# Optimization experiments

Hardware: AMD Instinct MI355X
Metric: run time of the kernel (lower is better)

## Reference

```python
import jax, jax.numpy as jnp
import numpy as np

N = 50000
E = 800000
HID = 128
H = 4
C = HID // H  # 32
ED = 4


def setup_inputs() -> dict:
    key = jax.random.key(0)
    ks = jax.random.split(key, 16)
    s = 0.05
    rn = lambda k, shape: jax.random.normal(k, shape, jnp.float32) * s
    z = lambda n: jnp.zeros((n,), jnp.float32)
    return {
        'x': jax.random.normal(ks[0], (N, HID), jnp.float32),
        'edge_index': jax.random.randint(ks[1], (2, E), 0, N, dtype=jnp.int32),
        'edge_attr': jax.random.normal(ks[2], (E, ED), jnp.float32),
        'ln1_g': jnp.ones((HID,), jnp.float32), 'ln1_b': z(HID),
        'Wq': rn(ks[3], (HID, HID)), 'bq': z(HID),
        'Wk': rn(ks[4], (HID, HID)), 'bk': z(HID),
        'Wv': rn(ks[5], (HID, HID)), 'bv': z(HID),
        'We': rn(ks[6], (HID, ED)),
        'Wskip': rn(ks[7], (HID, HID)), 'bskip': z(HID),
        'Wbeta': rn(ks[8], (1, 3 * HID)),
        'ln2_g': jnp.ones((HID,), jnp.float32), 'ln2_b': z(HID),
        'W1': rn(ks[9], (4 * HID, HID)), 'b1': z(4 * HID),
        'W2': rn(ks[10], (HID, 4 * HID)), 'b2': z(HID),
    }


def layer_norm(x, g, b, eps=1e-5):
    mu = jnp.mean(x, axis=-1, keepdims=True)
    var = jnp.mean(jnp.square(x - mu), axis=-1, keepdims=True)
    return (x - mu) * jax.lax.rsqrt(var + eps) * g + b


def transformer_conv(h, edge_index, edge_attr, Wq, bq, Wk, bk, Wv, bv, We, Wskip, bskip, Wbeta):
    src, dst = edge_index[0], edge_index[1]
    n = h.shape[0]
    q = (h @ Wq.T + bq).reshape(n, H, C)
    k = (h @ Wk.T + bk).reshape(n, H, C)
    v = (h @ Wv.T + bv).reshape(n, H, C)
    e = (edge_attr @ We.T).reshape(-1, H, C)  # [E,H,C]
    k_j = k[src] + e
    v_j = v[src] + e
    alpha = jnp.einsum('ehc,ehc->eh', q[dst], k_j) / np.sqrt(C)  # [E,H]
    # segment softmax over destination nodes
    m = jax.ops.segment_max(alpha, dst, num_segments=n)  # [N,H]
    a = jnp.exp(alpha - m[dst])
    denom = jax.ops.segment_sum(a, dst, num_segments=n) + 1e-16
    a = a / denom[dst]
    out = jax.ops.segment_sum(a[:, :, None] * v_j, dst, num_segments=n)  # [N,H,C]
    out = out.reshape(n, H * C)
    skip = h @ Wskip.T + bskip
    beta = jax.nn.sigmoid(jnp.concatenate([out, skip, out - skip], axis=-1) @ Wbeta.T)  # [N,1]
    return beta * skip + (1.0 - beta) * out


def reference(x, edge_index, edge_attr, ln1_g, ln1_b, Wq, bq, Wk, bk, Wv, bv, We, Wskip, bskip, Wbeta, ln2_g, ln2_b, W1, b1, W2, b2):
    h = transformer_conv(layer_norm(x, ln1_g, ln1_b), edge_index, edge_attr,
                         Wq, bq, Wk, bk, Wv, bv, We, Wskip, bskip, Wbeta)
    x = x + h
    h2 = layer_norm(x, ln2_g, ln2_b)
    h2 = jax.nn.relu(h2 @ W1.T + b1) @ W2.T + b2
    return x + h2
```

## Files before the change

kernel.cpp:

```cpp
#include <hip/hip_runtime.h>

#define N_NODES 50000
#define E_EDGES 800000
#define HID 128
#define NQB 782
#define SCAN_BLK 1024
#define NSB 49
#define WCB 192

typedef __attribute__((ext_vector_type(8))) short short8;
typedef __attribute__((ext_vector_type(4))) float f32x4;

static __device__ __forceinline__ unsigned short f2bf(float f) {
  unsigned int u = __builtin_bit_cast(unsigned int, f);
  u += 0x7fff + ((u >> 16) & 1);
  return (unsigned short)(u >> 16);
}
static __device__ __forceinline__ float bf2f(unsigned short u) {
  return __builtin_bit_cast(float, (unsigned int)u << 16);
}
static __device__ __forceinline__ unsigned short pk_fp8(float a, float b) {
  return (unsigned short)(__builtin_amdgcn_cvt_pk_fp8_f32(a, b, 0, false) & 0xffff);
}

__global__ __launch_bounds__(256) void wcvt_kernel(
    const float4* __restrict__ Wq, const float4* __restrict__ Wk,
    const float4* __restrict__ Wv, const float4* __restrict__ Ws,
    const float4* __restrict__ W1, const float4* __restrict__ W2,
    unsigned short* __restrict__ wqkvs, unsigned short* __restrict__ w1b,
    unsigned short* __restrict__ w2b, int* __restrict__ deg)
{
  if (blockIdx.x >= WCB) {
    int idx = ((blockIdx.x - WCB) * 256 + threadIdx.x) * 4;
    if (idx + 3 < N_NODES) *(int4*)(deg + idx) = (int4){0, 0, 0, 0};
    else {
      for (int t = 0; t < 4; t++)
        if (idx + t < N_NODES) deg[idx + t] = 0;
    }
    return;
  }
  int i = blockIdx.x * 256 + threadIdx.x;
  const float4* src;
  unsigned short* dst;
  if (i < 16384) {
    int part = i >> 12;
    src = ((part == 0) ? Wq : (part == 1) ? Wk : (part == 2) ? Wv : Ws) + (i & 4095);
    dst = wqkvs + i * 4;
  } else if (i < 32768) {
    src = W1 + (i - 16384); dst = w1b + (size_t)(i - 16384) * 4;
  } else {
    src = W2 + (i - 32768); dst = w2b + (size_t)(i - 32768) * 4;
  }
  float4 v = *src;
  ushort4 o;
  o.x = f2bf(v.x); o.y = f2bf(v.y); o.z = f2bf(v.z); o.w = f2bf(v.w);
  *(ushort4*)dst = o;
}

__global__ __launch_bounds__(256) void qkvs_kernel(
    const float* __restrict__ x,
    const float* __restrict__ g1, const float* __restrict__ bln,
    const unsigned short* __restrict__ wqkvs,
    const float* __restrict__ bq, const float* __restrict__ bk,
    const float* __restrict__ bv, const float* __restrict__ bs,
    unsigned short* __restrict__ qb, unsigned char* __restrict__ kvb,
    unsigned short* __restrict__ sb,
    const int* __restrict__ ei, int* __restrict__ deg, int n)
{
  if (blockIdx.x >= NQB) {
    for (int e = (blockIdx.x - NQB) * 256 + threadIdx.x; e < E_EDGES;
         e += NQB * 256)
      atomicAdd(deg + ei[E_EDGES + e], 1);
    return;
  }
  __shared__ short lnA[64][128];
  int node0 = blockIdx.x * 64;
  int tid = threadIdx.x;
  int g = tid >> 4, gl = tid & 15, c0 = gl * 8;
  {
    float gv[8], bv2[8];
    *(float4*)&gv[0] = *(const float4*)(g1 + c0);
    *(float4*)&gv[4] = *(const float4*)(g1 + c0 + 4);
    *(float4*)&bv2[0] = *(const float4*)(bln + c0);
    *(float4*)&bv2[4] = *(const float4*)(bln + c0 + 4);
    for (int ni = 0; ni < 4; ni++) {
      int nl = ni * 16 + g;
      int node = node0 + nl;
      short8 h8 = {0, 0, 0, 0, 0, 0, 0, 0};
      if (node < n) {
        float vals[8];
        const float* row = x + (size_t)node * HID + c0;
        *(float4*)&vals[0] = *(const float4*)row;
        *(float4*)&vals[4] = *(const float4*)(row + 4);
        float sum = 0.f;
        #pragma unroll
        for (int j = 0; j < 8; j++) sum += vals[j];
        sum += __shfl_xor(sum, 8); sum += __shfl_xor(sum, 4);
        sum += __shfl_xor(sum, 2); sum += __shfl_xor(sum, 1);
        float mu = sum * (1.f / 128.f);
        float sq = 0.f;
        #pragma unroll
        for (int j = 0; j < 8; j++) { float d = vals[j] - mu; sq += d * d; }
        sq += __shfl_xor(sq, 8); sq += __shfl_xor(sq, 4);
        sq += __shfl_xor(sq, 2); sq += __shfl_xor(sq, 1);
        float rstd = rsqrtf(sq * (1.f / 128.f) + 1e-5f);
        #pragma unroll
        for (int j = 0; j < 8; j++)
          h8[j] = (short)f2bf((vals[j] - mu) * rstd * gv[j] + bv2[j]);
      }
      *(short8*)&lnA[nl][(gl ^ (nl & 7)) * 8] = h8;
    }
  }
  __syncthreads();
  int w = tid >> 6, lane = tid & 63;
  int lg = lane >> 4, ll = lane & 15;
  short8 bfr[4][4];
  #pragma unroll
  for (int nt = 0; nt < 4; nt++) {
    int arow = nt * 16 + ll;
    #pragma unroll
    for (int kt = 0; kt < 4; kt++)
      bfr[nt][kt] = *(const short8*)&lnA[arow][((kt * 4 + lg) ^ (ll & 7)) * 8];
  }
  const float* biasp = (w == 0) ? bq : (w == 1) ? bk : (w == 2) ? bv : bs;
  bool ok[4];
  #pragma unroll
  for (int nt = 0; nt < 4; nt++) ok[nt] = (node0 + nt * 16 + ll) < n;
  for (int ci = 0; ci < 8; ci++) {
    const unsigned short* wrow = wqkvs + (size_t)(w * 128 + ci * 16 + ll) * 128 + lg * 8;
    short8 af[4];
    #pragma unroll
    for (int kt = 0; kt < 4; kt++) af[kt] = *(const short8*)(wrow + kt * 32);
    f32x4 acc[4];
    #pragma unroll
    for (int nt = 0; nt < 4; nt++) acc[nt] = (f32x4){0.f, 0.f, 0.f, 0.f};
    #pragma unroll
    for (int kt = 0; kt < 4; kt++)
      #pragma unroll
      for (int nt = 0; nt < 4; nt++)
        acc[nt] = __builtin_amdgcn_mfma_f32_16x16x32_bf16(af[kt], bfr[nt][kt], acc[nt], 0, 0, 0);
    int jj = ci * 16 + lg * 4;
    float4 bq4 = *(const float4*)(biasp + jj);
    #pragma unroll
    for (int nt = 0; nt < 4; nt++) {
      if (!ok[nt]) continue;
      int node = node0 + nt * 16 + ll;
      float v0 = acc[nt][0] + bq4.x, v1 = acc[nt][1] + bq4.y;
      float v2 = acc[nt][2] + bq4.z, v3 = acc[nt][3] + bq4.w;
      if (w == 0 || w == 3) {
        ushort4 o;
        o.x = f2bf(v0); o.y = f2bf(v1); o.z = f2bf(v2); o.w = f2bf(v3);
        *(ushort4*)((w == 0 ? qb : sb) + (size_t)node * HID + jj) = o;
      } else {
        unsigned word = (unsigned)pk_fp8(v0, v1) | ((unsigned)pk_fp8(v2, v3) << 16);
        *(unsigned*)(kvb + (unsigned)node * 256 + (jj >> 2) * 8 + (w == 1 ? 0 : 4)) = word;
      }
    }
  }
}

__global__ __launch_bounds__(256) void scan1_kernel(
    const int* __restrict__ deg, int* __restrict__ bsum)
{
  __shared__ int wsum[4];
  int b = blockIdx.x;
  int idx = b * SCAN_BLK + threadIdx.x * 4;
  int4 v = {0, 0, 0, 0};
  if (idx + 3 < N_NODES) v = *(const int4*)(deg + idx);
  else {
    if (idx     < N_NODES) v.x = deg[idx];
    if (idx + 1 < N_NODES) v.y = deg[idx + 1];
    if (idx + 2 < N_NODES) v.z = deg[idx + 2];
    if (idx + 3 < N_NODES) v.w = deg[idx + 3];
  }
  int s = v.x + v.y + v.z + v.w;
  for (int m = 1; m < 64; m <<= 1) s += __shfl_xor(s, m);
  int lane = threadIdx.x & 63, w = threadIdx.x >> 6;
  if (lane == 0) wsum[w] = s;
  __syncthreads();
  if (threadIdx.x == 0) bsum[b] = wsum[0] + wsum[1] + wsum[2] + wsum[3];
}

__global__ __launch_bounds__(256) void scan2_kernel(
    const int* __restrict__ deg, const int* __restrict__ bsum,
    int* __restrict__ row_start, int* __restrict__ cursor)
{
  __shared__ int boff_s;
  __shared__ int wsum[4];
  int b = blockIdx.x;
  int tid = threadIdx.x;
  int lane = tid & 63, w = tid >> 6;
  if (tid < 64) {
    int v = (lane < b) ? bsum[lane] : 0;
    for (int m = 1; m < 64; m <<= 1) v += __shfl_xor(v, m);
    if (lane == 0) boff_s = v;
  }
  int idx = b * SCAN_BLK + tid * 4;
  int4 v = {0, 0, 0, 0};
  if (idx + 3 < N_NODES) v = *(const int4*)(deg + idx);
  else {
    if (idx     < N_NODES) v.x = deg[idx];
    if (idx + 1 < N_NODES) v.y = deg[idx + 1];
    if (idx + 2 < N_NODES) v.z = deg[idx + 2];
    if (idx + 3 < N_NODES) v.w = deg[idx + 3];
  }
  int ts = v.x + v.y + v.z + v.w;
  int incl = ts;
  for (int m = 1; m < 64; m <<= 1) {
    int t = __shfl_up(incl, m);
    if (lane >= m) incl += t;
  }
  if (lane == 63) wsum[w] = incl;
  __syncthreads();
  int woff = 0;
  for (int i = 0; i < w; i++) woff += wsum[i];
  int excl = boff_s + woff + incl - ts;
  int4 o;
  o.x = excl;
  o.y = excl + v.x;
  o.z = excl + v.x + v.y;
  o.w = excl + v.x + v.y + v.z;
  if (idx + 3 < N_NODES) {
    *(int4*)(row_start + idx) = o;
    *(int4*)(cursor + idx) = o;
  } else {
    if (idx     < N_NODES) { row_start[idx]     = o.x; cursor[idx]     = o.x; }
    if (idx + 1 < N_NODES) { row_start[idx + 1] = o.y; cursor[idx + 1] = o.y; }
    if (idx + 2 < N_NODES) { row_start[idx + 2] = o.z; cursor[idx + 2] = o.z; }
    if (idx + 3 < N_NODES) { row_start[idx + 3] = o.w; cursor[idx + 3] = o.w; }
  }
}

__global__ __launch_bounds__(256) void scatter_kernel(
    const int* __restrict__ ei, const float4* __restrict__ attr,
    int* __restrict__ cursor,
    int* __restrict__ csr_src, float4* __restrict__ csr_attr)
{
  int e = blockIdx.x * 256 + threadIdx.x;
  if (e >= E_EDGES) return;
  int dst = ei[E_EDGES + e];
  int pos = atomicAdd(cursor + dst, 1);
  csr_src[pos] = ei[e] * 256;
  csr_attr[pos] = attr[e];
}

__global__ __launch_bounds__(256) void gather_kernel(
    const int* __restrict__ row_start, const int* __restrict__ deg,
    const int* __restrict__ csr_src, const float4* __restrict__ csr_attr,
    const float* __restrict__ We,
    const unsigned short* __restrict__ qb, const unsigned char* __restrict__ kvb,
    const float* __restrict__ x, const unsigned short* __restrict__ sb,
    const float* __restrict__ Wb, unsigned short* __restrict__ xnb, int n)
{
  int node = (blockIdx.x * blockDim.x + threadIdx.x) >> 6;
  if (node >= n) return;
  int lane = threadIdx.x & 63;
  int hl = lane & 31;
  int s  = lane >> 5;
  int c0 = hl * 4;
  ushort4 q4 = *(const ushort4*)(qb + (size_t)node * HID + c0);
  float q0 = bf2f(q4.x), q1 = bf2f(q4.y), q2 = bf2f(q4.z), q3 = bf2f(q4.w);
  float4 wr0 = *(const float4*)(We + (c0 + 0) * 4);
  float4 wr1 = *(const float4*)(We + (c0 + 1) * 4);
  float4 wr2 = *(const float4*)(We + (c0 + 2) * 4);
  float4 wr3 = *(const float4*)(We + (c0 + 3) * 4);
  float qwe0 = q0 * wr0.x + q1 * wr1.x + q2 * wr2.x + q3 * wr3.x;
  float qwe1 = q0 * wr0.y + q1 * wr1.y + q2 * wr2.y + q3 * wr3.y;
  float qwe2 = q0 * wr0.z + q1 * wr1.z + q2 * wr2.z + q3 * wr3.z;
  float qwe3 = q0 * wr0.w + q1 * wr1.w + q2 * wr2.w + q3 * wr3.w;
  qwe0 += __shfl_xor(qwe0, 1); qwe0 += __shfl_xor(qwe0, 2); qwe0 += __shfl_xor(qwe0, 4);
  qwe1 += __shfl_xor(qwe1, 1); qwe1 += __shfl_xor(qwe1, 2); qwe1 += __shfl_xor(qwe1, 4);
  qwe2 += __shfl_xor(qwe2, 1); qwe2 += __shfl_xor(qwe2, 2); qwe2 += __shfl_xor(qwe2, 4);
  qwe3 += __shfl_xor(qwe3, 1); qwe3 += __shfl_xor(qwe3, 2); qwe3 += __shfl_xor(qwe3, 4);
  const float s2 = 0.17677669529663687f * 1.4426950408889634f;
  float q0s = q0 * s2, q1s = q1 * s2, q2s = q2 * s2, q3s = q3 * s2;
  qwe0 *= s2; qwe1 *= s2; qwe2 *= s2; qwe3 *= s2;
  float acc0 = 0.f, acc1 = 0.f, acc2 = 0.f, acc3 = 0.f, den = 0.f;
  float aat0 = 0.f, aat1 = 0.f, aat2 = 0.f, aat3 = 0.f;
  int rs = row_start[node];
  int cnt = deg[node];
  int re = rs + cnt;
  unsigned off = (unsigned)hl * 8;
  uint2 kvc = {0u, 0u};
  float4 ac = {0.f, 0.f, 0.f, 0.f};
  {
    int jj = rs + s;
    if (jj < re) {
      kvc = *(const uint2*)(kvb + (unsigned)csr_src[jj] + off);
      ac = csr_attr[jj];
    }
  }
  for (int j = rs; j < re; j += 2) {
    uint2 kvn = {0u, 0u};
    float4 an = {0.f, 0.f, 0.f, 0.f};
    int jn = j + 2 + s;
    if (jn < re) {
      kvn = *(const uint2*)(kvb + (unsigned)csr_src[jn] + off);
      an = csr_attr[jn];
    }
    float dot = q0s * __builtin_amdgcn_cvt_f32_fp8((int)kvc.x, 0) +
                q1s * __builtin_amdgcn_cvt_f32_fp8((int)kvc.x, 1) +
                q2s * __builtin_amdgcn_cvt_f32_fp8((int)kvc.x, 2) +
                q3s * __builtin_amdgcn_cvt_f32_fp8((int)kvc.x, 3);
    dot += __shfl_xor(dot, 1);
    dot += __shfl_xor(dot, 2);
    dot += __shfl_xor(dot, 4);
    float e = exp2f(dot + qwe0 * ac.x + qwe1 * ac.y + qwe2 * ac.z + qwe3 * ac.w);
    e = (j + s < re) ? e : 0.f;
    den += e;
    aat0 += e * ac.x; aat1 += e * ac.y;
    aat2 += e * ac.z; aat3 += e * ac.w;
    acc0 += e * __builtin_amdgcn_cvt_f32_fp8((int)kvc.y, 0);
    acc1 += e * __builtin_amdgcn_cvt_f32_fp8((int)kvc.y, 1);
    acc2 += e * __builtin_amdgcn_cvt_f32_fp8((int)kvc.y, 2);
    acc3 += e * __builtin_amdgcn_cvt_f32_fp8((int)kvc.y, 3);
    kvc = kvn; ac = an;
  }
  acc0 += __shfl_xor(acc0, 32); acc1 += __shfl_xor(acc1, 32);
  acc2 += __shfl_xor(acc2, 32); acc3 += __shfl_xor(acc3, 32);
  den  += __shfl_xor(den, 32);
  aat0 += __shfl_xor(aat0, 32); aat1 += __shfl_xor(aat1, 32);
  aat2 += __shfl_xor(aat2, 32); aat3 += __shfl_xor(aat3, 32);
  float inv = 1.0f / (den + 1e-16f);
  float o0 = (acc0 + wr0.x * aat0 + wr0.y * aat1 + wr0.z * aat2 + wr0.w * aat3) * inv;
  float o1 = (acc1 + wr1.x * aat0 + wr1.y * aat1 + wr1.z * aat2 + wr1.w * aat3) * inv;
  float o2 = (acc2 + wr2.x * aat0 + wr2.y * aat1 + wr2.z * aat2 + wr2.w * aat3) * inv;
  float o3 = (acc3 + wr3.x * aat0 + wr3.y * aat1 + wr3.z * aat2 + wr3.w * aat3) * inv;
  ushort4 sp4 = *(const ushort4*)(sb + (size_t)node * HID + c0);
  float sk0 = bf2f(sp4.x), sk1 = bf2f(sp4.y), sk2 = bf2f(sp4.z), sk3 = bf2f(sp4.w);
  float4 wbA = *(const float4*)(Wb + c0);
  float4 wbB = *(const float4*)(Wb + 128 + c0);
  float4 wbC = *(const float4*)(Wb + 256 + c0);
  float bpart = o0 * (wbA.x + wbC.x) + sk0 * (wbB.x - wbC.x) +
                o1 * (wbA.y + wbC.y) + sk1 * (wbB.y - wbC.y) +
                o2 * (wbA.z + wbC.z) + sk2 * (wbB.z - wbC.z) +
                o3 * (wbA.w + wbC.w) + sk3 * (wbB.w - wbC.w);
  bpart += __shfl_xor(bpart, 1); bpart += __shfl_xor(bpart, 2);
  bpart += __shfl_xor(bpart, 4); bpart += __shfl_xor(bpart, 8);
  bpart += __shfl_xor(bpart, 16);
  float beta = 1.0f / (1.0f + exp2f(-bpart * 1.4426950408889634f));
  if (lane < 32) {
    float4 xv = *(const float4*)(x + (size_t)node * HID + c0);
    ushort4 o4;
    o4.x = f2bf(xv.x + beta * sk0 + (1.0f - beta) * o0);
    o4.y = f2bf(xv.y + beta * sk1 + (1.0f - beta) * o1);
    o4.z = f2bf(xv.z + beta * sk2 + (1.0f - beta) * o2);
    o4.w = f2bf(xv.w + beta * sk3 + (1.0f - beta) * o3);
    *(ushort4*)(xnb + (size_t)node * HID + c0) = o4;
  }
}

__global__ __launch_bounds__(256) void mlp_kernel(
    const unsigned short* __restrict__ xnb,
    const float* __restrict__ g2, const float* __restrict__ b2ln,
    const unsigned short* __restrict__ w1b, const float* __restrict__ b1,
    const unsigned short* __restrict__ w2b, const float* __restrict__ b2,
    float* __restrict__ out, int n)
{
  __shared__ short lnA[32][128];
  __shared__ short tS[32][512];
  short* tsf = &tS[0][0];
  int node0 = blockIdx.x * 32;
  int tid = threadIdx.x;
  int g = tid >> 4, gl = tid & 15, c0 = gl * 8;
  {
    float gv[8], bv2[8];
    *(float4*)&gv[0] = *(const float4*)(g2 + c0);
    *(float4*)&gv[4] = *(const float4*)(g2 + c0 + 4);
    *(float4*)&bv2[0] = *(const float4*)(b2ln + c0);
    *(float4*)&bv2[4] = *(const float4*)(b2ln + c0 + 4);
    for (int ni = 0; ni < 2; ni++) {
      int nl = ni * 16 + g;
      int node = node0 + nl;
      short8 h8 = {0, 0, 0, 0, 0, 0, 0, 0};
      if (node < n) {
        short8 raw = *(const short8*)(xnb + (size_t)node * HID + c0);
        float vals[8];
        #pragma unroll
        for (int j = 0; j < 8; j++) vals[j] = bf2f((unsigned short)raw[j]);
        float sum = 0.f;
        #pragma unroll
        for (int j = 0; j < 8; j++) sum += vals[j];
        sum += __shfl_xor(sum, 8); sum += __shfl_xor(sum, 4);
        sum += __shfl_xor(sum, 2); sum += __shfl_xor(sum, 1);
        float mu = sum * (1.f / 128.f);
        float sq = 0.f;
        #pragma unroll
        for (int j = 0; j < 8; j++) { float d = vals[j] - mu; sq += d * d; }
        sq += __shfl_xor(sq, 8); sq += __shfl_xor(sq, 4);
        sq += __shfl_xor(sq, 2); sq += __shfl_xor(sq, 1);
        float rstd = rsqrtf(sq * (1.f / 128.f) + 1e-5f);
        #pragma unroll
        for (int j = 0; j < 8; j++)
          h8[j] = (short)f2bf((vals[j] - mu) * rstd * gv[j] + bv2[j]);
      }
      *(short8*)&lnA[nl][(gl ^ (nl & 7)) * 8] = h8;
    }
  }
  __syncthreads();
  int w = tid >> 6, lane = tid & 63;
  int lg = lane >> 4, ll = lane & 15;
  int swz = (ll & 7) << 1;
  bool ok0 = (node0 + ll) < n, ok1 = (node0 + 16 + ll) < n;
  {
    short8 bfr1[2][4];
    #pragma unroll
    for (int nt = 0; nt < 2; nt++) {
      int arow = nt * 16 + ll;
      #pragma unroll
      for (int kt = 0; kt < 4; kt++)
        bfr1[nt][kt] = *(const short8*)&lnA[arow][((kt * 4 + lg) ^ (ll & 7)) * 8];
    }
    for (int ji = 0; ji < 8; ji++) {
      int jt = w * 8 + ji;
      const unsigned short* wrow = w1b + (size_t)(jt * 16 + ll) * 128 + lg * 8;
      short8 af[4];
      #pragma unroll
      for (int kt = 0; kt < 4; kt++) af[kt] = *(const short8*)(wrow + kt * 32);
      f32x4 acc[2];
      acc[0] = (f32x4){0.f, 0.f, 0.f, 0.f};
      acc[1] = (f32x4){0.f, 0.f, 0.f, 0.f};
      #pragma unroll
      for (int kt = 0; kt < 4; kt++) {
        acc[0] = __builtin_amdgcn_mfma_f32_16x16x32_bf16(af[kt], bfr1[0][kt], acc[0], 0, 0, 0);
        acc[1] = __builtin_amdgcn_mfma_f32_16x16x32_bf16(af[kt], bfr1[1][kt], acc[1], 0, 0, 0);
      }
      float4 bj = *(const float4*)(b1 + jt * 16 + lg * 4);
      int gr = jt * 4 + lg;
      #pragma unroll
      for (int nt = 0; nt < 2; nt++) {
        int nl = nt * 16 + ll;
        ushort4 o;
        o.x = f2bf(fmaxf(acc[nt][0] + bj.x, 0.f));
        o.y = f2bf(fmaxf(acc[nt][1] + bj.y, 0.f));
        o.z = f2bf(fmaxf(acc[nt][2] + bj.z, 0.f));
        o.w = f2bf(fmaxf(acc[nt][3] + bj.w, 0.f));
        *(ushort4*)&tsf[nl * 512 + (gr ^ swz) * 4] = o;
      }
    }
  }
  __syncthreads();
  {
    for (int ci = 0; ci < 2; ci++) {
      int ct = w * 2 + ci;
      f32x4 acc[2];
      acc[0] = (f32x4){0.f, 0.f, 0.f, 0.f};
      acc[1] = (f32x4){0.f, 0.f, 0.f, 0.f};
      const unsigned short* wrow = w2b + (size_t)(ct * 16 + ll) * 512 + lg * 8;
      #pragma unroll
      for (int kt = 0; kt < 16; kt++) {
        short8 af = *(const short8*)(wrow + kt * 32);
        int G = kt * 8 + lg * 2;
        short8 b0 = *(const short8*)&tsf[(0 * 16 + ll) * 512 + (G ^ swz) * 4];
        short8 b1f = *(const short8*)&tsf[(1 * 16 + ll) * 512 + (G ^ swz) * 4];
        acc[0] = __builtin_amdgcn_mfma_f32_16x16x32_bf16(af, b0, acc[0], 0, 0, 0);
        acc[1] = __builtin_amdgcn_mfma_f32_16x16x32_bf16(af, b1f, acc[1], 0, 0, 0);
      }
      int c = ct * 16 + lg * 4;
      float4 b2q = *(const float4*)(b2 + c);
      #pragma unroll
      for (int nt = 0; nt < 2; nt++) {
        if (nt == 0 ? !ok0 : !ok1) continue;
        int node = node0 + nt * 16 + ll;
        ushort4 xr = *(const ushort4*)(xnb + (size_t)node * HID + c);
        float4 o;
        o.x = bf2f(xr.x) + acc[nt][0] + b2q.x;
        o.y = bf2f(xr.y) + acc[nt][1] + b2q.y;
        o.z = bf2f(xr.z) + acc[nt][2] + b2q.z;
        o.w = bf2f(xr.w) + acc[nt][3] + b2q.w;
        *(float4*)(out + (size_t)node * HID + c) = o;
      }
    }
  }
}

extern "C" void kernel_launch(void* const* d_in, const int* in_sizes, int n_in,
                              void* d_out, int out_size, void* d_ws, size_t ws_size,
                              hipStream_t stream) {
  const float* x     = (const float*)d_in[0];
  const int*   ei    = (const int*)d_in[1];
  const float* attr  = (const float*)d_in[2];
  const float* ln1_g = (const float*)d_in[3];
  const float* ln1_b = (const float*)d_in[4];
  const float* Wq    = (const float*)d_in[5];
  const float* bq    = (const float*)d_in[6];
  const float* Wk    = (const float*)d_in[7];
  const float* bk    = (const float*)d_in[8];
  const float* Wv    = (const float*)d_in[9];
  const float* bv    = (const float*)d_in[10];
  const float* We    = (const float*)d_in[11];
  const float* Wskip = (const float*)d_in[12];
  const float* bskip = (const float*)d_in[13];
  const float* Wbeta = (const float*)d_in[14];
  const float* ln2_g = (const float*)d_in[15];
  const float* ln2_b = (const float*)d_in[16];
  const float* W1    = (const float*)d_in[17];
  const float* b1    = (const float*)d_in[18];
  const float* W2    = (const float*)d_in[19];
  const float* b2    = (const float*)d_in[20];
  float* out = (float*)d_out;
  float* ws  = (float*)d_ws;

  size_t NH  = (size_t)N_NODES * HID;
  size_t NHf = NH / 2;
  unsigned short* sb  = (unsigned short*)ws;
  unsigned short* xnb = (unsigned short*)(ws + NHf);
  unsigned short* qb  = (unsigned short*)(ws + 2 * NHf);
  unsigned char*  kvb = (unsigned char*)(ws + 3 * NHf);
  float* base2 = ws + 3 * NHf + (size_t)N_NODES * 256 / 4;
  int* deg       = (int*)base2;
  int* row_start = deg + N_NODES;
  int* cursor    = row_start + N_NODES;
  int* csr_src   = cursor + N_NODES;
  float4* csr_attr = (float4*)(base2 + 950000);
  unsigned short* wqkvs = (unsigned short*)(base2 + 950000 + (size_t)E_EDGES * 4);
  unsigned short* w1b   = wqkvs + 65536;
  unsigned short* w2b   = w1b + 65536;
  int* bsum = (int*)(w2b + 65536);

  wcvt_kernel<<<WCB + NSB, 256, 0, stream>>>(
      (const float4*)Wq, (const float4*)Wk, (const float4*)Wv,
      (const float4*)Wskip, (const float4*)W1, (const float4*)W2,
      wqkvs, w1b, w2b, deg);
  qkvs_kernel<<<2 * NQB, 256, 0, stream>>>(
      x, ln1_g, ln1_b, wqkvs, bq, bk, bv, bskip, qb, kvb, sb, ei, deg, N_NODES);
  scan1_kernel<<<NSB, 256, 0, stream>>>(deg, bsum);
  scan2_kernel<<<NSB, 256, 0, stream>>>(deg, bsum, row_start, cursor);
  scatter_kernel<<<(E_EDGES + 255) / 256, 256, 0, stream>>>(
      ei, (const float4*)attr, cursor, csr_src, csr_attr);
  gather_kernel<<<(N_NODES * 64 + 255) / 256, 256, 0, stream>>>(
      row_start, deg, csr_src, csr_attr, We, qb, kvb, x, sb, Wbeta, xnb, N_NODES);
  mlp_kernel<<<(N_NODES + 31) / 32, 256, 0, stream>>>(
      xnb, ln2_g, ln2_b, w1b, b1, w2b, b2, out, N_NODES);
}
```

Measured before the change: 248.8 us.

## Process four edges per wave with 16-lane groups and interleaved 8-channel KV layout

Changes the fp8 K/V buffer layout so each lane's 8 K channels and 8 V channels sit in one contiguous 16-byte chunk. The gather kernel now splits each wave into four 16-lane groups, each handling one edge with a 16-byte load and packed fp8 conversions. The goal is to raise memory-level parallelism per wave, cut loop iterations and the shuffle depth of the per-edge dot product. In exchange each lane holds more registers, and the final reductions across the edge groups need extra shuffles.

Result: slower. 297.3 us (+19.5%).

```diff
diff --git a/kernel.cpp b/kernel.cpp
--- a/kernel.cpp
+++ b/kernel.cpp
@@ -10,6 +10,7 @@
 
 typedef __attribute__((ext_vector_type(8))) short short8;
 typedef __attribute__((ext_vector_type(4))) float f32x4;
+typedef __attribute__((ext_vector_type(2))) float f32x2;
 
 static __device__ __forceinline__ unsigned short f2bf(float f) {
   unsigned int u = __builtin_bit_cast(unsigned int, f);
@@ -153,7 +154,8 @@
         *(ushort4*)((w == 0 ? qb : sb) + (size_t)node * HID + jj) = o;
       } else {
         unsigned word = (unsigned)pk_fp8(v0, v1) | ((unsigned)pk_fp8(v2, v3) << 16);
-        *(unsigned*)(kvb + (unsigned)node * 256 + (jj >> 2) * 8 + (w == 1 ? 0 : 4)) = word;
+        *(unsigned*)(kvb + (unsigned)node * 256 + (jj >> 3) * 16 + (jj & 7) +
+                     (w == 1 ? 0 : 8)) = word;
       }
     }
   }
@@ -255,98 +257,110 @@
   int node = (blockIdx.x * blockDim.x + threadIdx.x) >> 6;
   if (node >= n) return;
   int lane = threadIdx.x & 63;
-  int hl = lane & 31;
-  int s  = lane >> 5;
-  int c0 = hl * 4;
-  ushort4 q4 = *(const ushort4*)(qb + (size_t)node * HID + c0);
-  float q0 = bf2f(q4.x), q1 = bf2f(q4.y), q2 = bf2f(q4.z), q3 = bf2f(q4.w);
-  float4 wr0 = *(const float4*)(We + (c0 + 0) * 4);
-  float4 wr1 = *(const float4*)(We + (c0 + 1) * 4);
-  float4 wr2 = *(const float4*)(We + (c0 + 2) * 4);
-  float4 wr3 = *(const float4*)(We + (c0 + 3) * 4);
-  float qwe0 = q0 * wr0.x + q1 * wr1.x + q2 * wr2.x + q3 * wr3.x;
-  float qwe1 = q0 * wr0.y + q1 * wr1.y + q2 * wr2.y + q3 * wr3.y;
-  float qwe2 = q0 * wr0.z + q1 * wr1.z + q2 * wr2.z + q3 * wr3.z;
-  float qwe3 = q0 * wr0.w + q1 * wr1.w + q2 * wr2.w + q3 * wr3.w;
-  qwe0 += __shfl_xor(qwe0, 1); qwe0 += __shfl_xor(qwe0, 2); qwe0 += __shfl_xor(qwe0, 4);
-  qwe1 += __shfl_xor(qwe1, 1); qwe1 += __shfl_xor(qwe1, 2); qwe1 += __shfl_xor(qwe1, 4);
-  qwe2 += __shfl_xor(qwe2, 1); qwe2 += __shfl_xor(qwe2, 2); qwe2 += __shfl_xor(qwe2, 4);
-  qwe3 += __shfl_xor(qwe3, 1); qwe3 += __shfl_xor(qwe3, 2); qwe3 += __shfl_xor(qwe3, 4);
+  int hl = lane & 15;
+  int s  = lane >> 4;
+  int c0 = hl * 8;
+  short8 q8r = *(const short8*)(qb + (size_t)node * HID + c0);
+  float qv[8];
+  #pragma unroll
+  for (int i = 0; i < 8; i++) qv[i] = bf2f((unsigned short)q8r[i]);
+  float qwe0 = 0.f, qwe1 = 0.f, qwe2 = 0.f, qwe3 = 0.f;
+  #pragma unroll
+  for (int i = 0; i < 8; i++) {
+    float4 wr = *(const float4*)(We + (c0 + i) * 4);
+    qwe0 += qv[i] * wr.x; qwe1 += qv[i] * wr.y;
+    qwe2 += qv[i] * wr.z; qwe3 += qv[i] * wr.w;
+  }
+  qwe0 += __shfl_xor(qwe0, 1); qwe0 += __shfl_xor(qwe0, 2);
+  qwe1 += __shfl_xor(qwe1, 1); qwe1 += __shfl_xor(qwe1, 2);
+  qwe2 += __shfl_xor(qwe2, 1); qwe2 += __shfl_xor(qwe2, 2);
+  qwe3 += __shfl_xor(qwe3, 1); qwe3 += __shfl_xor(qwe3, 2);
   const float s2 = 0.17677669529663687f * 1.4426950408889634f;
-  float q0s = q0 * s2, q1s = q1 * s2, q2s = q2 * s2, q3s = q3 * s2;
+  float qs[8];
+  #pragma unroll
+  for (int i = 0; i < 8; i++) qs[i] = qv[i] * s2;
   qwe0 *= s2; qwe1 *= s2; qwe2 *= s2; qwe3 *= s2;
-  float acc0 = 0.f, acc1 = 0.f, acc2 = 0.f, acc3 = 0.f, den = 0.f;
+  float acc[8] = {0.f, 0.f, 0.f, 0.f, 0.f, 0.f, 0.f, 0.f};
+  float den = 0.f;
   float aat0 = 0.f, aat1 = 0.f, aat2 = 0.f, aat3 = 0.f;
   int rs = row_start[node];
   int cnt = deg[node];
   int re = rs + cnt;
-  unsigned off = (unsigned)hl * 8;
-  uint2 kvc = {0u, 0u};
+  unsigned off = (unsigned)hl * 16;
+  uint4 kvc = {0u, 0u, 0u, 0u};
   float4 ac = {0.f, 0.f, 0.f, 0.f};
   {
     int jj = rs + s;
     if (jj < re) {
-      kvc = *(const uint2*)(kvb + (unsigned)csr_src[jj] + off);
+      kvc = *(const uint4*)(kvb + (unsigned)csr_src[jj] + off);
       ac = csr_attr[jj];
     }
   }
-  for (int j = rs; j < re; j += 2) {
-    uint2 kvn = {0u, 0u};
+  for (int j = rs; j < re; j += 4) {
+    uint4 kvn = {0u, 0u, 0u, 0u};
     float4 an = {0.f, 0.f, 0.f, 0.f};
-    int jn = j + 2 + s;
+    int jn = j + 4 + s;
     if (jn < re) {
-      kvn = *(const uint2*)(kvb + (unsigned)csr_src[jn] + off);
+      kvn = *(const uint4*)(kvb + (unsigned)csr_src[jn] + off);
       an = csr_attr[jn];
     }
-    float dot = q0s * __builtin_amdgcn_cvt_f32_fp8((int)kvc.x, 0) +
-                q1s * __builtin_amdgcn_cvt_f32_fp8((int)kvc.x, 1) +
-                q2s * __builtin_amdgcn_cvt_f32_fp8((int)kvc.x, 2) +
-                q3s * __builtin_amdgcn_cvt_f32_fp8((int)kvc.x, 3);
+    f32x2 k01 = __builtin_amdgcn_cvt_pk_f32_fp8((int)kvc.x, false);
+    f32x2 k23 = __builtin_amdgcn_cvt_pk_f32_fp8((int)kvc.x, true);
+    f32x2 k45 = __builtin_amdgcn_cvt_pk_f32_fp8((int)kvc.y, false);
+    f32x2 k67 = __builtin_amdgcn_cvt_pk_f32_fp8((int)kvc.y, true);
+    float dot = qs[0] * k01.x + qs[1] * k01.y + qs[2] * k23.x + qs[3] * k23.y +
+                qs[4] * k45.x + qs[5] * k45.y + qs[6] * k67.x + qs[7] * k67.y;
     dot += __shfl_xor(dot, 1);
     dot += __shfl_xor(dot, 2);
-    dot += __shfl_xor(dot, 4);
     float e = exp2f(dot + qwe0 * ac.x + qwe1 * ac.y + qwe2 * ac.z + qwe3 * ac.w);
     e = (j + s < re) ? e : 0.f;
     den += e;
     aat0 += e * ac.x; aat1 += e * ac.y;
     aat2 += e * ac.z; aat3 += e * ac.w;
-    acc0 += e * __builtin_amdgcn_cvt_f32_fp8((int)kvc.y, 0);
-    acc1 += e * __builtin_amdgcn_cvt_f32_fp8((int)kvc.y, 1);
-    acc2 += e * __builtin_amdgcn_cvt_f32_fp8((int)kvc.y, 2);
-    acc3 += e * __builtin_amdgcn_cvt_f32_fp8((int)kvc.y, 3);
+    f32x2 v01 = __builtin_amdgcn_cvt_pk_f32_fp8((int)kvc.z, false);
+    f32x2 v23 = __builtin_amdgcn_cvt_pk_f32_fp8((int)kvc.z, true);
+    f32x2 v45 = __builtin_amdgcn_cvt_pk_f32_fp8((int)kvc.w, false);
+    f32x2 v67 = __builtin_amdgcn_cvt_pk_f32_fp8((int)kvc.w, true);
+    acc[0] += e * v01.x; acc[1] += e * v01.y;
+    acc[2] += e * v23.x; acc[3] += e * v23.y;
+    acc[4] += e * v45.x; acc[5] += e * v45.y;
+    acc[6] += e * v67.x; acc[7] += e * v67.y;
     kvc = kvn; ac = an;
   }
-  acc0 += __shfl_xor(acc0, 32); acc1 += __shfl_xor(acc1, 32);
-  acc2 += __shfl_xor(acc2, 32); acc3 += __shfl_xor(acc3, 32);
-  den  += __shfl_xor(den, 32);
-  aat0 += __shfl_xor(aat0, 32); aat1 += __shfl_xor(aat1, 32);
-  aat2 += __shfl_xor(aat2, 32); aat3 += __shfl_xor(aat3, 32);
+  #pragma unroll
+  for (int i = 0; i < 8; i++) {
+    acc[i] += __shfl_xor(acc[i], 16);
+    acc[i] += __shfl_xor(acc[i], 32);
+  }
+  den += __shfl_xor(den, 16); den += __shfl_xor(den, 32);
+  aat0 += __shfl_xor(aat0, 16); aat0 += __shfl_xor(aat0, 32);
+  aat1 += __shfl_xor(aat1, 16); aat1 += __shfl_xor(aat1, 32);
+  aat2 += __shfl_xor(aat2, 16); aat2 += __shfl_xor(aat2, 32);
+  aat3 += __shfl_xor(aat3, 16); aat3 += __shfl_xor(aat3, 32);
   float inv = 1.0f / (den + 1e-16f);
-  float o0 = (acc0 + wr0.x * aat0 + wr0.y * aat1 + wr0.z * aat2 + wr0.w * aat3) * inv;
-  float o1 = (acc1 + wr1.x * aat0 + wr1.y * aat1 + wr1.z * aat2 + wr1.w * aat3) * inv;
-  float o2 = (acc2 + wr2.x * aat0 + wr2.y * aat1 + wr2.z * aat2 + wr2.w * aat3) * inv;
-  float o3 = (acc3 + wr3.x * aat0 + wr3.y * aat1 + wr3.z * aat2 + wr3.w * aat3) * inv;
-  ushort4 sp4 = *(const ushort4*)(sb + (size_t)node * HID + c0);
-  float sk0 = bf2f(sp4.x), sk1 = bf2f(sp4.y), sk2 = bf2f(sp4.z), sk3 = bf2f(sp4.w);
-  float4 wbA = *(const float4*)(Wb + c0);
-  float4 wbB = *(const float4*)(Wb + 128 + c0);
-  float4 wbC = *(const float4*)(Wb + 256 + c0);
-  float bpart = o0 * (wbA.x + wbC.x) + sk0 * (wbB.x - wbC.x) +
-                o1 * (wbA.y + wbC.y) + sk1 * (wbB.y - wbC.y) +
-                o2 * (wbA.z + wbC.z) + sk2 * (wbB.z - wbC.z) +
-                o3 * (wbA.w + wbC.w) + sk3 * (wbB.w - wbC.w);
+  float o[8], sk[8];
+  short8 spr = *(const short8*)(sb + (size_t)node * HID + c0);
+  float bpart = 0.f;
+  #pragma unroll
+  for (int i = 0; i < 8; i++) {
+    float4 wr = *(const float4*)(We + (c0 + i) * 4);
+    o[i] = (acc[i] + wr.x * aat0 + wr.y * aat1 + wr.z * aat2 + wr.w * aat3) * inv;
+    sk[i] = bf2f((unsigned short)spr[i]);
+    int c = c0 + i;
+    bpart += o[i] * (Wb[c] + Wb[256 + c]) + sk[i] * (Wb[128 + c] - Wb[256 + c]);
+  }
   bpart += __shfl_xor(bpart, 1); bpart += __shfl_xor(bpart, 2);
   bpart += __shfl_xor(bpart, 4); bpart += __shfl_xor(bpart, 8);
-  bpart += __shfl_xor(bpart, 16);
   float beta = 1.0f / (1.0f + exp2f(-bpart * 1.4426950408889634f));
-  if (lane < 32) {
-    float4 xv = *(const float4*)(x + (size_t)node * HID + c0);
-    ushort4 o4;
-    o4.x = f2bf(xv.x + beta * sk0 + (1.0f - beta) * o0);
-    o4.y = f2bf(xv.y + beta * sk1 + (1.0f - beta) * o1);
-    o4.z = f2bf(xv.z + beta * sk2 + (1.0f - beta) * o2);
-    o4.w = f2bf(xv.w + beta * sk3 + (1.0f - beta) * o3);
-    *(ushort4*)(xnb + (size_t)node * HID + c0) = o4;
+  if (lane < 16) {
+    float xv[8];
+    *(float4*)&xv[0] = *(const float4*)(x + (size_t)node * HID + c0);
+    *(float4*)&xv[4] = *(const float4*)(x + (size_t)node * HID + c0 + 4);
+    short8 o8;
+    #pragma unroll
+    for (int i = 0; i < 8; i++)
+      o8[i] = (short)f2bf(xv[i] + beta * sk[i] + (1.0f - beta) * o[i]);
+    *(short8*)(xnb + (size_t)node * HID + c0) = o8;
   }
 }
 
```
